# Performance work log

Hardware: AMD Instinct MI355X
Metric: run time of the kernel (lower is better)

Reference implementation:

```python
import jax, jax.numpy as jnp
import numpy as np

B, T, C, H = 8, 2048, 1024, 128

def setup_inputs() -> dict:
    key = jax.random.key(0)
    k1, k2, k3, k4 = jax.random.split(key, 4)
    scale = 0.02
    return {
        "x": jax.random.normal(k1, (B, T, C), dtype=jnp.float32),
        "Wq": jax.random.normal(k2, (C, H), dtype=jnp.float32) * scale,
        "Wk": jax.random.normal(k3, (C, H), dtype=jnp.float32) * scale,
        "Wv": jax.random.normal(k4, (C, H), dtype=jnp.float32) * scale,
    }

def reference(x, Wq, Wk, Wv):
    # Single causal attention head (dropout p=0.0 -> identity)
    q = jnp.einsum('btc,ch->bth', x, Wq)
    k = jnp.einsum('btc,ch->bth', x, Wk)
    v = jnp.einsum('btc,ch->bth', x, Wv)
    head_size = k.shape[-1]
    scores = jnp.einsum('bth,bsh->bts', q, k) / jnp.sqrt(jnp.asarray(head_size, q.dtype))  # [B,T,T]
    causal = jnp.tril(jnp.ones((scores.shape[1], scores.shape[2]), dtype=bool))
    scores = jnp.where(causal, scores, -jnp.inf)
    weights = jax.nn.softmax(scores, axis=-1)
    context = jnp.einsum('bts,bsh->bth', weights, v)  # [B,T,H]
    return context
```

## Files before the change

### kernel.cpp

```cpp
#include <hip/hip_runtime.h>

typedef __bf16 bf16x8 __attribute__((ext_vector_type(8)));
typedef float f32x4 __attribute__((ext_vector_type(4)));
typedef float fv4 __attribute__((ext_vector_type(4)));

#define B_ 8
#define T_ 2048
#define C_ 1024
#define H_ 128

__device__ __forceinline__ void gload16(void* lds, const void* g) {
  __builtin_amdgcn_global_load_lds(
      (const __attribute__((address_space(1))) void*)g,
      (__attribute__((address_space(3))) void*)lds, 16, 0, 0);
}


__global__ __launch_bounds__(256) void prep_kernel(
    const float* __restrict__ Wq, const float* __restrict__ Wk,
    const float* __restrict__ Wv, __bf16* __restrict__ Wt)
{
  __shared__ __bf16 ldsT[128 * 136];
  const int tid = threadIdx.x;
  const int k0 = blockIdx.x * 128;
  const int wsel = blockIdx.y;
  const float* W = wsel == 0 ? Wq : (wsel == 1 ? Wk : Wv);
#pragma unroll
  for (int i = 0; i < 16; ++i) {
    int fidx = tid + 256 * i;
    int k = fidx >> 5, h4 = (fidx & 31) << 2;
    fv4 w = *(const fv4*)(W + (size_t)(k0 + k) * H_ + h4);
#pragma unroll
    for (int j = 0; j < 4; ++j) ldsT[(h4 + j) * 136 + k] = (__bf16)w[j];
  }
  __syncthreads();
#pragma unroll
  for (int i = 0; i < 8; ++i) {
    int sidx = tid + 256 * i;
    int h = sidx >> 4, c8 = (sidx & 15) << 3;
    *(bf16x8*)(Wt + (size_t)wsel * H_ * C_ + (size_t)h * C_ + k0 + c8) =
        *(const bf16x8*)&ldsT[h * 136 + c8];
  }
}

__global__ __launch_bounds__(256) void proj_kernel(
    const float* __restrict__ x, const __bf16* __restrict__ Wt,
    __bf16* __restrict__ Qw, __bf16* __restrict__ Kw, __bf16* __restrict__ Vtw)
{
  __shared__ __align__(16) float ldsA[2][64 * 64];
  __shared__ __align__(16) __bf16 ldsB[2][192 * 64];
  const int tid = threadIdx.x;
  const int wave = tid >> 6, lane = tid & 63;
  const int q4 = lane >> 4, l16 = lane & 15;
  const int wm = wave >> 1, wn = wave & 1;
  const int bt0 = blockIdx.x * 64;
  const int cb0 = blockIdx.y * 192;

  const int arow16 = tid >> 4, agx = tid & 15;
  const int bcol32 = tid >> 3, bgx = tid & 7;

  const f32x4 zero4 = {0.f, 0.f, 0.f, 0.f};
  f32x4 acc[2][6];
#pragma unroll
  for (int mt = 0; mt < 2; ++mt)
#pragma unroll
    for (int nt = 0; nt < 6; ++nt) acc[mt][nt] = zero4;

  auto stage = [&](int bufi, int k0) {
#pragma unroll
    for (int i = 0; i < 4; ++i) {
      int row = i * 16 + arow16;
      gload16((char*)&ldsA[bufi][0] + i * 4096 + wave * 1024,
              x + (size_t)(bt0 + row) * C_ + k0 + ((agx ^ (row & 7)) << 2));
    }
#pragma unroll
    for (int i = 0; i < 6; ++i) {
      int col = i * 32 + bcol32;
      gload16((char*)&ldsB[bufi][0] + i * 4096 + wave * 1024,
              Wt + (size_t)(cb0 + col) * C_ + k0 + ((bgx ^ (col & 7)) << 3));
    }
  };

  stage(0, 0);
  stage(1, 64);

  for (int it = 0; it < 16; ++it) {
    const int buf = it & 1;
    if (it < 15) asm volatile("s_waitcnt vmcnt(10)" ::: "memory");
    else         asm volatile("s_waitcnt vmcnt(0)" ::: "memory");
    __builtin_amdgcn_sched_barrier(0);
    __builtin_amdgcn_s_barrier();
    __builtin_amdgcn_sched_barrier(0);
#pragma unroll
    for (int kc = 0; kc < 2; ++kc) {
      bf16x8 af[2];
#pragma unroll
      for (int mt = 0; mt < 2; ++mt) {
        const int rl = wm * 32 + mt * 16 + l16;
        const int rx = rl & 7;
        fv4 a0 = *(const fv4*)&ldsA[buf][rl * 64 + (((kc * 8 + q4 * 2 + 0) ^ rx) << 2)];
        fv4 a1 = *(const fv4*)&ldsA[buf][rl * 64 + (((kc * 8 + q4 * 2 + 1) ^ rx) << 2)];
#pragma unroll
        for (int j = 0; j < 4; ++j) { af[mt][j] = (__bf16)a0[j]; af[mt][4 + j] = (__bf16)a1[j]; }
      }
#pragma unroll
      for (int nt = 0; nt < 6; ++nt) {
        const int cl = wn * 96 + nt * 16 + l16;
        bf16x8 bf = *(const bf16x8*)&ldsB[buf][cl * 64 + (((kc * 4 + q4) ^ (cl & 7)) << 3)];
#pragma unroll
        for (int mt = 0; mt < 2; ++mt)
          acc[mt][nt] = __builtin_amdgcn_mfma_f32_16x16x32_bf16(af[mt], bf, acc[mt][nt], 0, 0, 0);
      }
    }
    __builtin_amdgcn_sched_barrier(0);
    __builtin_amdgcn_s_barrier();
    __builtin_amdgcn_sched_barrier(0);
    if (it + 2 < 16) stage(buf, (it + 2) * 64);
  }

  const int b = bt0 >> 11, t0 = bt0 & (T_ - 1);
  __bf16* ldsV = (__bf16*)&ldsB[0][0];
#pragma unroll
  for (int mt = 0; mt < 2; ++mt)
#pragma unroll
    for (int nt = 0; nt < 6; ++nt) {
      int gcol = cb0 + wn * 96 + nt * 16 + l16;
#pragma unroll
      for (int r = 0; r < 4; ++r) {
        int tl = wm * 32 + mt * 16 + q4 * 4 + r;
        float v = acc[mt][nt][r];
        if (gcol < 128) Qw[(size_t)(bt0 + tl) * H_ + gcol] = (__bf16)v;
        else if (gcol < 256) Kw[(size_t)(bt0 + tl) * H_ + (gcol - 128)] = (__bf16)v;
        else ldsV[(gcol - 256) * 72 + tl] = (__bf16)v;
      }
    }
  if (cb0 == 192) {
    __syncthreads();
#pragma unroll
    for (int i = 0; i < 4; ++i) {
      int idx = tid + 256 * i;
      int h = idx >> 3, t8 = (idx & 7) << 3;
      *(bf16x8*)(Vtw + ((size_t)b * H_ + h) * T_ + t0 + t8) =
          *(const bf16x8*)&ldsV[h * 72 + t8];
    }
  }
}

__global__ __launch_bounds__(256) void attn_split(
    const __bf16* __restrict__ Q, const __bf16* __restrict__ K,
    const __bf16* __restrict__ Vt, __bf16* __restrict__ PO,
    float* __restrict__ Pl, float* __restrict__ out)
{
  __shared__ __align__(16) __bf16 ldsK[2][64 * 128];
  __shared__ __align__(16) __bf16 ldsV[2][128 * 64];
  __shared__ __align__(16) __bf16 ldsP[4][16 * 72];
  const int tid = threadIdx.x;
  const int wave = tid >> 6, lane = tid & 63;
  const int q4 = lane >> 4, l16 = lane & 15;
  const int b = blockIdx.y;
  int rem = blockIdx.x, qb = 0;
  while (rem >= (qb >> 3) + 1) { rem -= (qb >> 3) + 1; ++qb; }
  const int c = rem;
  const int tstart = c << 3;
  const int tend = min(tstart + 8, qb + 1);
  const int nch = (qb >> 3) + 1;
  const int qw = qb * 64 + wave * 16;
  const __bf16* Qb = Q + (size_t)b * T_ * H_;
  const __bf16* Kb = K + (size_t)b * T_ * H_;
  const __bf16* Vb = Vt + (size_t)b * H_ * T_;
  __bf16* ldsPw = &ldsP[wave][0];

  bf16x8 qf[4];
#pragma unroll
  for (int kc = 0; kc < 4; ++kc)
    qf[kc] = *(const bf16x8*)(Qb + (size_t)(qw + l16) * H_ + kc * 32 + q4 * 8);

  const f32x4 zero4 = {0.f, 0.f, 0.f, 0.f};
  f32x4 o[8];
#pragma unroll
  for (int nt = 0; nt < 8; ++nt) o[nt] = zero4;
  float lsum[4] = {0.f, 0.f, 0.f, 0.f};

  auto stageKV = [&](int bufi, int t) {
    const int kv0 = t << 6;
#pragma unroll
    for (int i = 0; i < 4; ++i) {
      int kr = i * 16 + (tid >> 4);
      gload16((char*)&ldsK[bufi][0] + i * 4096 + wave * 1024,
              Kb + (size_t)(kv0 + kr) * H_ + (((tid & 15) ^ (kr & 7)) << 3));
      int vr = i * 32 + (tid >> 3);
      gload16((char*)&ldsV[bufi][0] + i * 4096 + wave * 1024,
              Vb + (size_t)vr * T_ + kv0 + (((tid & 7) ^ (vr & 7)) << 3));
    }
  };

  stageKV(0, tstart);
  if (tstart + 1 < tend) stageKV(1, tstart + 1);

  for (int t = tstart; t < tend; ++t) {
    const int buf = (t - tstart) & 1;
    const int kv0 = t << 6;
    if (t + 1 < tend) asm volatile("s_waitcnt vmcnt(8)" ::: "memory");
    else              asm volatile("s_waitcnt vmcnt(0)" ::: "memory");
    __builtin_amdgcn_sched_barrier(0);
    __builtin_amdgcn_s_barrier();
    __builtin_amdgcn_sched_barrier(0);

    f32x4 s[4];
#pragma unroll
    for (int nt = 0; nt < 4; ++nt) s[nt] = zero4;
#pragma unroll
    for (int nt = 0; nt < 4; ++nt) {
      const int krow = nt * 16 + l16;
      const int kx = krow & 7;
#pragma unroll
      for (int kc = 0; kc < 4; ++kc) {
        bf16x8 kf = *(const bf16x8*)&ldsK[buf][krow * 128 + (((kc * 4 + q4) ^ kx) << 3)];
        s[nt] = __builtin_amdgcn_mfma_f32_16x16x32_bf16(qf[kc], kf, s[nt], 0, 0, 0);
      }
    }

    if (t == qb) {
#pragma unroll
      for (int r = 0; r < 4; ++r) {
        const int grow = qw + q4 * 4 + r;
#pragma unroll
        for (int nt = 0; nt < 4; ++nt) {
          int col = kv0 + nt * 16 + l16;
          float p = (col <= grow) ? __expf(s[nt][r] * 0.08838834764831845f) : 0.f;
          lsum[r] += p;
          ldsPw[(q4 * 4 + r) * 72 + nt * 16 + l16] = (__bf16)p;
        }
      }
    } else {
#pragma unroll
      for (int r = 0; r < 4; ++r)
#pragma unroll
        for (int nt = 0; nt < 4; ++nt) {
          float p = __expf(s[nt][r] * 0.08838834764831845f);
          lsum[r] += p;
          ldsPw[(q4 * 4 + r) * 72 + nt * 16 + l16] = (__bf16)p;
        }
    }
#pragma unroll
    for (int kc2 = 0; kc2 < 2; ++kc2) {
      bf16x8 pf = *(const bf16x8*)&ldsPw[l16 * 72 + kc2 * 32 + q4 * 8];
#pragma unroll
      for (int nt = 0; nt < 8; ++nt) {
        const int vrow = nt * 16 + l16;
        bf16x8 vf = *(const bf16x8*)&ldsV[buf][vrow * 64 + (((kc2 * 4 + q4) ^ (vrow & 7)) << 3)];
        o[nt] = __builtin_amdgcn_mfma_f32_16x16x32_bf16(pf, vf, o[nt], 0, 0, 0);
      }
    }
    __builtin_amdgcn_sched_barrier(0);
    __builtin_amdgcn_s_barrier();
    __builtin_amdgcn_sched_barrier(0);
    if (t + 2 < tend) stageKV(buf, t + 2);
  }

  float lred[4];
#pragma unroll
  for (int r = 0; r < 4; ++r) {
    float l = lsum[r];
    l += __shfl_xor(l, 1);
    l += __shfl_xor(l, 2);
    l += __shfl_xor(l, 4);
    l += __shfl_xor(l, 8);
    lred[r] = l;
  }

  if (nch == 1) {
#pragma unroll
    for (int r = 0; r < 4; ++r) lred[r] = 1.f / lred[r];
#pragma unroll
    for (int nt = 0; nt < 8; ++nt)
#pragma unroll
      for (int r = 0; r < 4; ++r) {
        int row = qw + q4 * 4 + r;
        out[((size_t)b * T_ + row) * H_ + nt * 16 + l16] = o[nt][r] * lred[r];
      }
  } else {
    const int slot = b * 80 + qb + max(qb - 8, 0) + max(qb - 16, 0) + max(qb - 24, 0) + c;
    __bf16* POs = PO + (size_t)slot * 8192;
#pragma unroll
    for (int nt = 0; nt < 8; ++nt)
#pragma unroll
      for (int r = 0; r < 4; ++r)
        POs[(wave * 16 + q4 * 4 + r) * 128 + nt * 16 + l16] = (__bf16)o[nt][r];
    if (l16 == 0)
#pragma unroll
      for (int r = 0; r < 4; ++r)
        Pl[slot * 64 + wave * 16 + q4 * 4 + r] = lred[r];
  }
}

__global__ __launch_bounds__(256) void attn_combine(
    const __bf16* __restrict__ PO, const float* __restrict__ Pl,
    float* __restrict__ out)
{
  const int qb = 8 + (blockIdx.x >> 2);
  const int seg = blockIdx.x & 3;
  const int b = blockIdx.y;
  const int nch = (qb >> 3) + 1;
  const int slot0 = b * 80 + qb + max(qb - 8, 0) + max(qb - 16, 0) + max(qb - 24, 0);
  const int tid = threadIdx.x;
  const int rloc = seg * 16 + (tid >> 4);
  const int col8 = (tid & 15) << 3;
  float oacc[8] = {0.f};
  float lacc = 0.f;
  for (int cc = 0; cc < nch; ++cc) {
    const int slot = slot0 + cc;
    lacc += Pl[slot * 64 + rloc];
    bf16x8 v = *(const bf16x8*)(PO + (size_t)slot * 8192 + rloc * 128 + col8);
#pragma unroll
    for (int j = 0; j < 8; ++j) oacc[j] += (float)v[j];
  }
  const float inv = 1.f / lacc;
  float* op = out + ((size_t)b * T_ + qb * 64 + rloc) * H_ + col8;
  fv4 v0, v1;
#pragma unroll
  for (int j = 0; j < 4; ++j) { v0[j] = oacc[j] * inv; v1[j] = oacc[4 + j] * inv; }
  *(fv4*)op = v0;
  *(fv4*)(op + 4) = v1;
}

__global__ __launch_bounds__(256) void attn_mono(
    const __bf16* __restrict__ Q, const __bf16* __restrict__ K,
    const __bf16* __restrict__ Vt, float* __restrict__ out)
{
  __shared__ __align__(16) __bf16 ldsK[64 * 136];
  __shared__ __align__(16) __bf16 ldsV[128 * 72];
  __shared__ __align__(16) __bf16 ldsP[4][16 * 72];
  const int tid = threadIdx.x;
  const int wave = tid >> 6, lane = tid & 63;
  const int q4 = lane >> 4, l16 = lane & 15;
  const int qb = blockIdx.x, b = blockIdx.y;
  const int qw = qb * 64 + wave * 16;
  const __bf16* Qb = Q + (size_t)b * T_ * H_;
  const __bf16* Kb = K + (size_t)b * T_ * H_;
  const __bf16* Vb = Vt + (size_t)b * H_ * T_;
  __bf16* ldsPw = &ldsP[wave][0];

  bf16x8 qf[4];
#pragma unroll
  for (int kc = 0; kc < 4; ++kc)
    qf[kc] = *(const bf16x8*)(Qb + (size_t)(qw + l16) * H_ + kc * 32 + q4 * 8);

  const f32x4 zero4 = {0.f, 0.f, 0.f, 0.f};
  f32x4 o[8];
#pragma unroll
  for (int nt = 0; nt < 8; ++nt) o[nt] = zero4;
  float lsum[4] = {0.f, 0.f, 0.f, 0.f};
  const int ntile = qb + 1;

  bf16x8 kp[4], vp[4];
#pragma unroll
  for (int i = 0; i < 4; ++i) {
    int idx = tid + 256 * i;
    int krow = idx >> 4, kcol8 = (idx & 15) << 3;
    kp[i] = *(const bf16x8*)(Kb + (size_t)krow * H_ + kcol8);
    int vrow = idx >> 3, vcol8 = (idx & 7) << 3;
    vp[i] = *(const bf16x8*)(Vb + (size_t)vrow * T_ + vcol8);
  }

  for (int t = 0; t < ntile; ++t) {
    const int kv0 = t << 6;
#pragma unroll
    for (int i = 0; i < 4; ++i) {
      int idx = tid + 256 * i;
      int krow = idx >> 4, kcol8 = (idx & 15) << 3;
      *(bf16x8*)&ldsK[krow * 136 + kcol8] = kp[i];
      int vrow = idx >> 3, vcol8 = (idx & 7) << 3;
      *(bf16x8*)&ldsV[vrow * 72 + vcol8] = vp[i];
    }
    __syncthreads();
    int kvn = (t + 1 < ntile) ? (kv0 + 64) : kv0;
#pragma unroll
    for (int i = 0; i < 4; ++i) {
      int idx = tid + 256 * i;
      int krow = idx >> 4, kcol8 = (idx & 15) << 3;
      kp[i] = *(const bf16x8*)(Kb + (size_t)(kvn + krow) * H_ + kcol8);
      int vrow = idx >> 3, vcol8 = (idx & 7) << 3;
      vp[i] = *(const bf16x8*)(Vb + (size_t)vrow * T_ + kvn + vcol8);
    }
    f32x4 s[4];
#pragma unroll
    for (int nt = 0; nt < 4; ++nt) s[nt] = zero4;
#pragma unroll
    for (int nt = 0; nt < 4; ++nt)
#pragma unroll
      for (int kc = 0; kc < 4; ++kc) {
        bf16x8 kf = *(const bf16x8*)&ldsK[(nt * 16 + l16) * 136 + kc * 32 + q4 * 8];
        s[nt] = __builtin_amdgcn_mfma_f32_16x16x32_bf16(qf[kc], kf, s[nt], 0, 0, 0);
      }
#pragma unroll
    for (int r = 0; r < 4; ++r) {
      const int grow = qw + q4 * 4 + r;
#pragma unroll
      for (int nt = 0; nt < 4; ++nt) {
        int col = kv0 + nt * 16 + l16;
        float p = (col <= grow) ? __expf(s[nt][r] * 0.08838834764831845f) : 0.f;
        lsum[r] += p;
        ldsPw[(q4 * 4 + r) * 72 + nt * 16 + l16] = (__bf16)p;
      }
    }
#pragma unroll
    for (int kc2 = 0; kc2 < 2; ++kc2) {
      bf16x8 pf = *(const bf16x8*)&ldsPw[l16 * 72 + kc2 * 32 + q4 * 8];
#pragma unroll
      for (int nt = 0; nt < 8; ++nt) {
        bf16x8 vf = *(const bf16x8*)&ldsV[(nt * 16 + l16) * 72 + kc2 * 32 + q4 * 8];
        o[nt] = __builtin_amdgcn_mfma_f32_16x16x32_bf16(pf, vf, o[nt], 0, 0, 0);
      }
    }
    __syncthreads();
  }
  float rinv[4];
#pragma unroll
  for (int r = 0; r < 4; ++r) {
    float l = lsum[r];
    l += __shfl_xor(l, 1);
    l += __shfl_xor(l, 2);
    l += __shfl_xor(l, 4);
    l += __shfl_xor(l, 8);
    rinv[r] = 1.f / l;
  }
#pragma unroll
  for (int nt = 0; nt < 8; ++nt)
#pragma unroll
    for (int r = 0; r < 4; ++r) {
      int row = qw + q4 * 4 + r;
      out[((size_t)b * T_ + row) * H_ + nt * 16 + l16] = o[nt][r] * rinv[r];
    }
}

extern "C" void kernel_launch(void* const* d_in, const int* in_sizes, int n_in,
                              void* d_out, int out_size, void* d_ws, size_t ws_size,
                              hipStream_t stream) {
  const float* x  = (const float*)d_in[0];
  const float* Wq = (const float*)d_in[1];
  const float* Wk = (const float*)d_in[2];
  const float* Wv = (const float*)d_in[3];
  __bf16* ws = (__bf16*)d_ws;
  __bf16* Qw  = ws;
  __bf16* Kw  = ws + (size_t)B_ * T_ * H_;
  __bf16* Vtw = ws + (size_t)2 * B_ * T_ * H_;
  __bf16* Wt  = ws + (size_t)3 * B_ * T_ * H_;
  const size_t bf16_elems = 6684672;
  __bf16* PO = ws + bf16_elems;
  float* Pl = (float*)(ws + bf16_elems + (size_t)640 * 8192);
  const size_t need = bf16_elems * 2 + (size_t)640 * 8192 * 2 + (size_t)640 * 64 * 4;
  float* out = (float*)d_out;

  prep_kernel<<<dim3(8, 3), 256, 0, stream>>>(Wq, Wk, Wv, Wt);
  proj_kernel<<<dim3(256, 2), 256, 0, stream>>>(x, Wt, Qw, Kw, Vtw);
  if (ws_size >= need) {
    attn_split<<<dim3(80, 8), 256, 0, stream>>>(Qw, Kw, Vtw, PO, Pl, out);
    attn_combine<<<dim3(96, 8), 256, 0, stream>>>(PO, Pl, out);
  } else {
    attn_mono<<<dim3(32, 8), 256, 0, stream>>>(Qw, Kw, Vtw, out);
  }
}
```

Baseline: 157.7 us.

## Halve attention KV tile to 32 keys and interleave batches in flat grid

The split attention kernel now processes 32-key sub-tiles instead of 64, halving K/V/P LDS footprint and per-step register use while doubling the number of pipeline iterations, with a new swizzle for the 32-wide V tile. Both split and combine kernels switch to a 1D grid with batch in the low bits, so consecutive workgroups cover different batches at the same query block and the heavy-work distribution across CUs is balanced. The smaller LDS footprint aims to raise occupancy, at the cost of more barriers and waitcnts per unit of work.

New measurement: 152.4 us. 1.03x faster.

```diff
diff --git a/kernel.cpp b/kernel.cpp
--- a/kernel.cpp
+++ b/kernel.cpp
@@ -151,18 +151,20 @@
     const __bf16* __restrict__ Vt, __bf16* __restrict__ PO,
     float* __restrict__ Pl, float* __restrict__ out)
 {
-  __shared__ __align__(16) __bf16 ldsK[2][64 * 128];
-  __shared__ __align__(16) __bf16 ldsV[2][128 * 64];
-  __shared__ __align__(16) __bf16 ldsP[4][16 * 72];
+  __shared__ __align__(16) __bf16 ldsK[2][32 * 128];
+  __shared__ __align__(16) __bf16 ldsV[2][128 * 32];
+  __shared__ __align__(16) __bf16 ldsP[4][16 * 40];
   const int tid = threadIdx.x;
   const int wave = tid >> 6, lane = tid & 63;
   const int q4 = lane >> 4, l16 = lane & 15;
-  const int b = blockIdx.y;
-  int rem = blockIdx.x, qb = 0;
+  const int flat = blockIdx.x;
+  const int b = flat & 7;
+  int rem = flat >> 3, qb = 0;
   while (rem >= (qb >> 3) + 1) { rem -= (qb >> 3) + 1; ++qb; }
   const int c = rem;
   const int tstart = c << 3;
   const int tend = min(tstart + 8, qb + 1);
+  const int nst = 2 * (tend - tstart);
   const int nch = (qb >> 3) + 1;
   const int qw = qb * 64 + wave * 16;
   const __bf16* Qb = Q + (size_t)b * T_ * H_;
@@ -181,81 +183,79 @@
   for (int nt = 0; nt < 8; ++nt) o[nt] = zero4;
   float lsum[4] = {0.f, 0.f, 0.f, 0.f};
 
-  auto stageKV = [&](int bufi, int t) {
-    const int kv0 = t << 6;
-#pragma unroll
-    for (int i = 0; i < 4; ++i) {
-      int kr = i * 16 + (tid >> 4);
+  auto stageKV = [&](int bufi, int kv0) {
+#pragma unroll
+    for (int i = 0; i < 2; ++i) {
+      int idx = tid + 256 * i;
+      int kr = idx >> 4, kg = idx & 15;
       gload16((char*)&ldsK[bufi][0] + i * 4096 + wave * 1024,
-              Kb + (size_t)(kv0 + kr) * H_ + (((tid & 15) ^ (kr & 7)) << 3));
-      int vr = i * 32 + (tid >> 3);
+              Kb + (size_t)(kv0 + kr) * H_ + ((kg ^ (kr & 7)) << 3));
+      int vr = idx >> 2, vg = idx & 3;
       gload16((char*)&ldsV[bufi][0] + i * 4096 + wave * 1024,
-              Vb + (size_t)vr * T_ + kv0 + (((tid & 7) ^ (vr & 7)) << 3));
+              Vb + (size_t)vr * T_ + kv0 + ((vg ^ ((vr >> 1) & 3)) << 3));
     }
   };
 
-  stageKV(0, tstart);
-  if (tstart + 1 < tend) stageKV(1, tstart + 1);
-
-  for (int t = tstart; t < tend; ++t) {
-    const int buf = (t - tstart) & 1;
-    const int kv0 = t << 6;
-    if (t + 1 < tend) asm volatile("s_waitcnt vmcnt(8)" ::: "memory");
+  const int kvbase = tstart << 6;
+  stageKV(0, kvbase);
+  stageKV(1, kvbase + 32);
+
+  for (int ht = 0; ht < nst; ++ht) {
+    const int buf = ht & 1;
+    const int kv0 = kvbase + ht * 32;
+    if (ht + 1 < nst) asm volatile("s_waitcnt vmcnt(4)" ::: "memory");
     else              asm volatile("s_waitcnt vmcnt(0)" ::: "memory");
     __builtin_amdgcn_sched_barrier(0);
     __builtin_amdgcn_s_barrier();
     __builtin_amdgcn_sched_barrier(0);
 
-    f32x4 s[4];
-#pragma unroll
-    for (int nt = 0; nt < 4; ++nt) s[nt] = zero4;
-#pragma unroll
-    for (int nt = 0; nt < 4; ++nt) {
-      const int krow = nt * 16 + l16;
+    f32x4 s[2];
+    s[0] = zero4; s[1] = zero4;
+#pragma unroll
+    for (int nt2 = 0; nt2 < 2; ++nt2) {
+      const int krow = nt2 * 16 + l16;
       const int kx = krow & 7;
 #pragma unroll
       for (int kc = 0; kc < 4; ++kc) {
         bf16x8 kf = *(const bf16x8*)&ldsK[buf][krow * 128 + (((kc * 4 + q4) ^ kx) << 3)];
-        s[nt] = __builtin_amdgcn_mfma_f32_16x16x32_bf16(qf[kc], kf, s[nt], 0, 0, 0);
-      }
-    }
-
-    if (t == qb) {
+        s[nt2] = __builtin_amdgcn_mfma_f32_16x16x32_bf16(qf[kc], kf, s[nt2], 0, 0, 0);
+      }
+    }
+
+    if ((kv0 >> 6) == qb) {
 #pragma unroll
       for (int r = 0; r < 4; ++r) {
         const int grow = qw + q4 * 4 + r;
 #pragma unroll
-        for (int nt = 0; nt < 4; ++nt) {
-          int col = kv0 + nt * 16 + l16;
-          float p = (col <= grow) ? __expf(s[nt][r] * 0.08838834764831845f) : 0.f;
+        for (int nt2 = 0; nt2 < 2; ++nt2) {
+          int col = kv0 + nt2 * 16 + l16;
+          float p = (col <= grow) ? __expf(s[nt2][r] * 0.08838834764831845f) : 0.f;
           lsum[r] += p;
-          ldsPw[(q4 * 4 + r) * 72 + nt * 16 + l16] = (__bf16)p;
+          ldsPw[(q4 * 4 + r) * 40 + nt2 * 16 + l16] = (__bf16)p;
         }
       }
     } else {
 #pragma unroll
       for (int r = 0; r < 4; ++r)
 #pragma unroll
-        for (int nt = 0; nt < 4; ++nt) {
-          float p = __expf(s[nt][r] * 0.08838834764831845f);
+        for (int nt2 = 0; nt2 < 2; ++nt2) {
+          float p = __expf(s[nt2][r] * 0.08838834764831845f);
           lsum[r] += p;
-          ldsPw[(q4 * 4 + r) * 72 + nt * 16 + l16] = (__bf16)p;
+          ldsPw[(q4 * 4 + r) * 40 + nt2 * 16 + l16] = (__bf16)p;
         }
     }
-#pragma unroll
-    for (int kc2 = 0; kc2 < 2; ++kc2) {
-      bf16x8 pf = *(const bf16x8*)&ldsPw[l16 * 72 + kc2 * 32 + q4 * 8];
-#pragma unroll
-      for (int nt = 0; nt < 8; ++nt) {
-        const int vrow = nt * 16 + l16;
-        bf16x8 vf = *(const bf16x8*)&ldsV[buf][vrow * 64 + (((kc2 * 4 + q4) ^ (vrow & 7)) << 3)];
-        o[nt] = __builtin_amdgcn_mfma_f32_16x16x32_bf16(pf, vf, o[nt], 0, 0, 0);
-      }
+
+    bf16x8 pf = *(const bf16x8*)&ldsPw[l16 * 40 + q4 * 8];
+#pragma unroll
+    for (int nt = 0; nt < 8; ++nt) {
+      const int vrow = nt * 16 + l16;
+      bf16x8 vf = *(const bf16x8*)&ldsV[buf][vrow * 32 + ((q4 ^ ((vrow >> 1) & 3)) << 3)];
+      o[nt] = __builtin_amdgcn_mfma_f32_16x16x32_bf16(pf, vf, o[nt], 0, 0, 0);
     }
     __builtin_amdgcn_sched_barrier(0);
     __builtin_amdgcn_s_barrier();
     __builtin_amdgcn_sched_barrier(0);
-    if (t + 2 < tend) stageKV(buf, t + 2);
+    if (ht + 2 < nst) stageKV(buf, kv0 + 64);
   }
 
   float lred[4];
@@ -298,9 +298,11 @@
     const __bf16* __restrict__ PO, const float* __restrict__ Pl,
     float* __restrict__ out)
 {
-  const int qb = 8 + (blockIdx.x >> 2);
-  const int seg = blockIdx.x & 3;
-  const int b = blockIdx.y;
+  const int flat = blockIdx.x;
+  const int b = flat & 7;
+  const int rest = flat >> 3;
+  const int qb = 8 + (rest >> 2);
+  const int seg = rest & 3;
   const int nch = (qb >> 3) + 1;
   const int slot0 = b * 80 + qb + max(qb - 8, 0) + max(qb - 16, 0) + max(qb - 24, 0);
   const int tid = threadIdx.x;
@@ -455,8 +457,8 @@
   prep_kernel<<<dim3(8, 3), 256, 0, stream>>>(Wq, Wk, Wv, Wt);
   proj_kernel<<<dim3(256, 2), 256, 0, stream>>>(x, Wt, Qw, Kw, Vtw);
   if (ws_size >= need) {
-    attn_split<<<dim3(80, 8), 256, 0, stream>>>(Qw, Kw, Vtw, PO, Pl, out);
-    attn_combine<<<dim3(96, 8), 256, 0, stream>>>(PO, Pl, out);
+    attn_split<<<640, 256, 0, stream>>>(Qw, Kw, Vtw, PO, Pl, out);
+    attn_combine<<<768, 256, 0, stream>>>(PO, Pl, out);
   } else {
     attn_mono<<<dim3(32, 8), 256, 0, stream>>>(Qw, Kw, Vtw, out);
   }
```
